# Kernel tuning notes

Measured on AMD Instinct MI355X. Metric: run time of the kernel, lower is better.

The kernel has to match this reference:

```python
import jax, jax.numpy as jnp
import numpy as np


def setup_inputs() -> dict:
    key = jax.random.key(0)
    k1, k2, k3, k4 = jax.random.split(key, 4)
    B, C, h, w = 16, 512, 96, 96
    nodes, hidden, out_c = 7, 256, 512  # out_c must equal C (final view)
    inp = jax.random.normal(k1, (1, B, nodes, hidden), dtype=jnp.float32)
    res_feature = jax.random.normal(k2, (B, C, h, w), dtype=jnp.float32)
    # learned params (xavier-ish scale)
    node_fea = jax.random.normal(k3, (C + hidden, 1), dtype=jnp.float32) * 0.05
    weight = jax.random.normal(k4, (hidden, out_c), dtype=jnp.float32) * 0.05
    return {"input": inp, "res_feature": res_feature, "node_fea": node_fea, "weight": weight}


def reference(input, res_feature, node_fea, weight):
    # input: [1, B, nodes, hidden]; res_feature: [B, C, h, w]
    B, C, h, w = res_feature.shape
    _, _, nodes, hidden = input.shape
    HW = h * w
    x = input[0]  # [B, nodes, hidden]

    # res_feature -> [B, HW, C]
    res_view = res_feature.reshape(B, C, HW).transpose(0, 2, 1)

    # The original concatenates broadcasted [B,HW,nodes,C] and [B,HW,nodes,hidden]
    # then matmuls with node_fea [C+hidden, 1]. That factors exactly into:
    #   score[b,p,n] = res_view[b,p,:] @ node_fea[:C] + x[b,n,:] @ node_fea[C:]
    nf_res = node_fea[:C, 0]    # [C]
    nf_node = node_fea[C:, 0]   # [hidden]
    score_pix = jnp.einsum('bpc,c->bp', res_view, nf_res)   # [B, HW]
    score_node = jnp.einsum('bnh,h->bn', x, nf_node)        # [B, nodes]
    logits = score_pix[:, :, None] + score_node[:, None, :]  # [B, HW, nodes]

    attn = jax.nn.softmax(logits, axis=-1)  # softmax over nodes

    node_w = jnp.einsum('bnh,ho->bno', x, weight)           # [B, nodes, out_c]
    feat = jnp.einsum('bpn,bno->bpo', attn, node_w)         # [B, HW, out_c]

    feat = feat.transpose(0, 2, 1).reshape(B, C, h, w)      # out_c == C
    return jax.nn.relu(feat)
```

## Files before the change

### kernel.cpp

```cpp
#include <hip/hip_runtime.h>


#define NB      16
#define NC      512
#define NHW     9216
#define NODES   7
#define HIDDEN  256
#define OUTC    512

__global__ __launch_bounds__(256) void compute_v_kernel(
    const float* __restrict__ x,
    const float* __restrict__ node_fea,
    const float* __restrict__ weight,
    float* __restrict__ v)
{
    const int b = blockIdx.x;
    const int t = threadIdx.x;

    __shared__ float s_y[HIDDEN];
    __shared__ float s_attn[NODES];
    __shared__ float s_red[4];

    const float* xb = x + (size_t)b * NODES * HIDDEN;
    const float nf = node_fea[NC + t];

    for (int n = 0; n < NODES; n++) {
        float p = xb[n * HIDDEN + t] * nf;
        #pragma unroll
        for (int off = 32; off >= 1; off >>= 1) p += __shfl_down(p, off, 64);
        if ((t & 63) == 0) s_red[t >> 6] = p;
        __syncthreads();
        if (t == 0) s_attn[n] = s_red[0] + s_red[1] + s_red[2] + s_red[3];
        __syncthreads();
    }

    if (t == 0) {
        float m = s_attn[0];
        #pragma unroll
        for (int n = 1; n < NODES; n++) m = fmaxf(m, s_attn[n]);
        float e[NODES];
        float sum = 0.f;
        #pragma unroll
        for (int n = 0; n < NODES; n++) { e[n] = __expf(s_attn[n] - m); sum += e[n]; }
        float inv = 1.f / sum;
        #pragma unroll
        for (int n = 0; n < NODES; n++) s_attn[n] = e[n] * inv;
    }
    __syncthreads();

    float y = 0.f;
    #pragma unroll
    for (int n = 0; n < NODES; n++) y += s_attn[n] * xb[n * HIDDEN + t];
    s_y[t] = y;
    __syncthreads();

    float acc0 = 0.f, acc1 = 0.f;
    for (int h = 0; h < HIDDEN; h++) {
        const float yh = s_y[h];
        acc0 += yh * weight[h * OUTC + t];
        acc1 += yh * weight[h * OUTC + t + 256];
    }
    v[b * OUTC + t]       = fmaxf(acc0, 0.f);
    v[b * OUTC + t + 256] = fmaxf(acc1, 0.f);
}

__global__ __launch_bounds__(256) void broadcast_kernel(
    const float* __restrict__ v, float* __restrict__ out)
{
    const int row = blockIdx.x;
    const float val = v[row];
    const float4 f4 = make_float4(val, val, val, val);
    float4* o4 = reinterpret_cast<float4*>(out) + (size_t)row * (NHW / 4);
    #pragma unroll
    for (int i = 0; i < 9; i++)
        o4[threadIdx.x + i * 256] = f4;
}

extern "C" void kernel_launch(void* const* d_in, const int* in_sizes, int n_in,
                              void* d_out, int out_size, void* d_ws, size_t ws_size,
                              hipStream_t stream) {
    const float* x        = (const float*)d_in[0];
    const float* node_fea = (const float*)d_in[2];
    const float* weight   = (const float*)d_in[3];
    float* out = (float*)d_out;
    float* v   = (float*)d_ws;

    compute_v_kernel<<<NB, 256, 0, stream>>>(x, node_fea, weight, v);
    broadcast_kernel<<<NB * OUTC, 256, 0, stream>>>(v, out);
}
```

Baseline: 451.8 us.

## Fuse node attention, projection and broadcast into one kernel with nontemporal stores

Merges the small per-batch projection kernel and the broadcast kernel into a single launch. Each output-row block now recomputes the 7-node softmax and one 256-long dot product against a weight column before writing its broadcast row. The goal is to remove the serial 16-block prologue kernel, its workspace round-trip and the second launch. Output stores become nontemporal to avoid polluting the cache on the large write stream. The cost is redundant per-block recomputation and strided, uncoalesced weight reads.

```diff
diff --git a/kernel.cpp b/kernel.cpp
--- a/kernel.cpp
+++ b/kernel.cpp
@@ -8,72 +8,78 @@
 #define HIDDEN  256
 #define OUTC    512
 
-__global__ __launch_bounds__(256) void compute_v_kernel(
+typedef float v4f __attribute__((ext_vector_type(4)));
+
+__global__ __launch_bounds__(256) void fused_kernel(
     const float* __restrict__ x,
     const float* __restrict__ node_fea,
     const float* __restrict__ weight,
-    float* __restrict__ v)
+    float* __restrict__ out)
 {
-    const int b = blockIdx.x;
-    const int t = threadIdx.x;
+    const int row = blockIdx.x;
+    const int b   = row >> 9;
+    const int o   = row & 511;
+    const int t   = threadIdx.x;
+    const int lane = t & 63;
+    const int wv   = t >> 6;
 
-    __shared__ float s_y[HIDDEN];
-    __shared__ float s_attn[NODES];
-    __shared__ float s_red[4];
+    __shared__ float s_part[4][NODES];
+    __shared__ float s_vpart[4];
+    __shared__ float s_v;
 
     const float* xb = x + (size_t)b * NODES * HIDDEN;
     const float nf = node_fea[NC + t];
 
+    float xv[NODES];
+    float p[NODES];
+    #pragma unroll
     for (int n = 0; n < NODES; n++) {
-        float p = xb[n * HIDDEN + t] * nf;
+        xv[n] = xb[n * HIDDEN + t];
+        p[n]  = xv[n] * nf;
+    }
+    #pragma unroll
+    for (int off = 32; off >= 1; off >>= 1) {
         #pragma unroll
-        for (int off = 32; off >= 1; off >>= 1) p += __shfl_down(p, off, 64);
-        if ((t & 63) == 0) s_red[t >> 6] = p;
-        __syncthreads();
-        if (t == 0) s_attn[n] = s_red[0] + s_red[1] + s_red[2] + s_red[3];
-        __syncthreads();
+        for (int n = 0; n < NODES; n++) p[n] += __shfl_down(p[n], off, 64);
     }
-
-    if (t == 0) {
-        float m = s_attn[0];
+    if (lane == 0) {
         #pragma unroll
-        for (int n = 1; n < NODES; n++) m = fmaxf(m, s_attn[n]);
-        float e[NODES];
-        float sum = 0.f;
-        #pragma unroll
-        for (int n = 0; n < NODES; n++) { e[n] = __expf(s_attn[n] - m); sum += e[n]; }
-        float inv = 1.f / sum;
-        #pragma unroll
-        for (int n = 0; n < NODES; n++) s_attn[n] = e[n] * inv;
+        for (int n = 0; n < NODES; n++) s_part[wv][n] = p[n];
     }
     __syncthreads();
 
+    float sc[NODES];
+    #pragma unroll
+    for (int n = 0; n < NODES; n++)
+        sc[n] = s_part[0][n] + s_part[1][n] + s_part[2][n] + s_part[3][n];
+    float m = sc[0];
+    #pragma unroll
+    for (int n = 1; n < NODES; n++) m = fmaxf(m, sc[n]);
+    float sum = 0.f;
+    #pragma unroll
+    for (int n = 0; n < NODES; n++) { sc[n] = __expf(sc[n] - m); sum += sc[n]; }
+    const float inv = 1.f / sum;
+
     float y = 0.f;
     #pragma unroll
-    for (int n = 0; n < NODES; n++) y += s_attn[n] * xb[n * HIDDEN + t];
-    s_y[t] = y;
+    for (int n = 0; n < NODES; n++) y += sc[n] * xv[n];
+    y *= inv;
+
+    float vp = y * weight[t * OUTC + o];
+    #pragma unroll
+    for (int off = 32; off >= 1; off >>= 1) vp += __shfl_down(vp, off, 64);
+    if (lane == 0) s_vpart[wv] = vp;
+    __syncthreads();
+    if (t == 0)
+        s_v = fmaxf(s_vpart[0] + s_vpart[1] + s_vpart[2] + s_vpart[3], 0.f);
     __syncthreads();
 
-    float acc0 = 0.f, acc1 = 0.f;
-    for (int h = 0; h < HIDDEN; h++) {
-        const float yh = s_y[h];
-        acc0 += yh * weight[h * OUTC + t];
-        acc1 += yh * weight[h * OUTC + t + 256];
-    }
-    v[b * OUTC + t]       = fmaxf(acc0, 0.f);
-    v[b * OUTC + t + 256] = fmaxf(acc1, 0.f);
-}
-
-__global__ __launch_bounds__(256) void broadcast_kernel(
-    const float* __restrict__ v, float* __restrict__ out)
-{
-    const int row = blockIdx.x;
-    const float val = v[row];
-    const float4 f4 = make_float4(val, val, val, val);
-    float4* o4 = reinterpret_cast<float4*>(out) + (size_t)row * (NHW / 4);
+    const float val = s_v;
+    const v4f f4 = { val, val, val, val };
+    v4f* o4 = reinterpret_cast<v4f*>(out) + (size_t)row * (NHW / 4);
     #pragma unroll
     for (int i = 0; i < 9; i++)
-        o4[threadIdx.x + i * 256] = f4;
+        __builtin_nontemporal_store(f4, &o4[t + i * 256]);
 }
 
 extern "C" void kernel_launch(void* const* d_in, const int* in_sizes, int n_in,
@@ -83,8 +89,6 @@
     const float* node_fea = (const float*)d_in[2];
     const float* weight   = (const float*)d_in[3];
     float* out = (float*)d_out;
-    float* v   = (float*)d_ws;
 
-    compute_v_kernel<<<NB, 256, 0, stream>>>(x, node_fea, weight, v);
-    broadcast_kernel<<<NB * OUTC, 256, 0, stream>>>(v, out);
+    fused_kernel<<<NB * OUTC, 256, 0, stream>>>(x, node_fea, weight, out);
 }
```

Result: faster. 429.6 us (-4.9%).
